# Kernel optimization log

Measured on AMD Instinct MI355X. Metric: run time of the kernel, lower is better.

The kernel has to match this reference:

```python
import jax, jax.numpy as jnp
import numpy as np

N_NODES = 50000      # nodes
N_EDGES = 800000     # edges (avg degree 16)
D = 128              # input_dim == hidden_dim
C = 32               # output_dim (classes)
G = 64               # number of graphs in batch
EPS = 1e-5           # LayerNorm eps (torch default)
NUM_LAYERS = 3


def setup_inputs() -> dict:
    key = jax.random.key(0)
    ks = jax.random.split(key, 12)
    scale = 1.0 / np.sqrt(D)
    x = jax.random.normal(ks[0], (N_NODES, D), dtype=jnp.float32)
    edge_index = jax.random.randint(ks[1], (2, N_EDGES), 0, N_NODES)
    batch = jnp.sort(jax.random.randint(ks[2], (N_NODES,), 0, G))
    # CustomConv params: self-loop linear + message linear, 3 layers stacked
    W_self = jax.random.normal(ks[3], (NUM_LAYERS, D, D), dtype=jnp.float32) * scale
    b_self = jnp.zeros((NUM_LAYERS, D), dtype=jnp.float32)
    W_msg = jax.random.normal(ks[4], (NUM_LAYERS, D, D), dtype=jnp.float32) * scale
    b_msg = jnp.zeros((NUM_LAYERS, D), dtype=jnp.float32)
    # two LayerNorms (after layers 0 and 1)
    ln_g = jnp.ones((2, D), dtype=jnp.float32)
    ln_b = jnp.zeros((2, D), dtype=jnp.float32)
    # post-MP MLP head: Linear(D,D) -> Dropout(identity in eval) -> Linear(D,C)
    W1 = jax.random.normal(ks[5], (D, D), dtype=jnp.float32) * scale
    b1 = jnp.zeros((D,), dtype=jnp.float32)
    W2 = jax.random.normal(ks[6], (D, C), dtype=jnp.float32) * scale
    b2 = jnp.zeros((C,), dtype=jnp.float32)
    return {"x": x, "W_self": W_self, "b_self": b_self, "W_msg": W_msg,
            "b_msg": b_msg, "ln_g": ln_g, "ln_b": ln_b, "W1": W1, "b1": b1,
            "W2": W2, "b2": b2, "edge_index": edge_index, "batch": batch}


def _layer_norm(h, g, b):
    mu = jnp.mean(h, axis=-1, keepdims=True)
    var = jnp.mean(jnp.square(h - mu), axis=-1, keepdims=True)
    return g * (h - mu) * jax.lax.rsqrt(var + EPS) + b


def reference(x, W_self, b_self, W_msg, b_msg, ln_g, ln_b, W1, b1, W2, b2,
              edge_index, batch):
    src, dst = edge_index[0], edge_index[1]
    for i in range(NUM_LAYERS):
        # CustomConv: self linear + sum-aggregated neighbor messages
        msg = x @ W_msg[i] + b_msg[i]                     # [N, D]
        agg = jax.ops.segment_sum(msg[src], dst, num_segments=N_NODES)
        x = x @ W_self[i] + b_self[i] + agg               # [N, D]
        x = jax.nn.relu(x)
        # dropout p=0.25 is identity in eval mode
        if i != NUM_LAYERS - 1:
            x = _layer_norm(x, ln_g[i], ln_b[i])
    # global mean pool over graphs
    sums = jax.ops.segment_sum(x, batch, num_segments=G)          # [G, D]
    cnt = jax.ops.segment_sum(jnp.ones((N_NODES,), x.dtype), batch,
                              num_segments=G)                     # [G]
    pooled = sums / jnp.maximum(cnt, 1.0)[:, None]
    # post-MP head (dropout identity in eval)
    h = pooled @ W1 + b1
    logits = h @ W2 + b2                                          # [G, C]
    return jax.nn.log_softmax(logits, axis=1)
```

## Files before the change

### kernel.cpp

```cpp
#include <hip/hip_runtime.h>
#include <hip/hip_bf16.h>
#include <math.h>

#define N_NODES 50000
#define N_EDGES 800000
#define DIM 128
#define CLS 32
#define NGRAPH 64
#define LN_EPS 1e-5f
#define CSR_CAP (N_EDGES + 8 * N_NODES)
#define NBLK 196
#define ABLK 128
#define EPB (N_EDGES / ABLK)
#define EB_STRIDE 7168
#define LCAP 8192
#define PSPLIT 16

typedef __attribute__((ext_vector_type(8))) short bf16x8;
typedef __attribute__((ext_vector_type(4))) float f32x4;

static __device__ __forceinline__ int lower_bound_i(const int* a, int n, int key) {
    int lo = 0, hi = n;
    while (lo < hi) { int mid = (lo + hi) >> 1; if (a[mid] < key) lo = mid + 1; else hi = mid; }
    return lo;
}


__global__ __launch_bounds__(256) void prep_kernel(
    const float* __restrict__ x, const float* __restrict__ Wself,
    const float* __restrict__ Wmsg, __hip_bfloat16* __restrict__ XbIn,
    __hip_bfloat16* __restrict__ WT,
    int* __restrict__ ecur, float* __restrict__ gsum,
    __hip_bfloat16* __restrict__ padA, __hip_bfloat16* __restrict__ padB,
    __hip_bfloat16* __restrict__ padC, __hip_bfloat16* __restrict__ padD) {
    int i = blockIdx.x * 256 + threadIdx.x;
    if (i < N_NODES * DIM / 2) {
        float2 v = ((const float2*)x)[i];
        ((__hip_bfloat162*)XbIn)[i] = __float22bfloat162_rn(v);
    }
    if (i < 3 * 128 * 256) {
        int l = i / (128 * 256);
        int rem = i - l * (128 * 256);
        int n = rem >> 8;
        int k = rem & 255;
        float v = (k < 128) ? Wself[l * 16384 + k * 128 + n]
                            : Wmsg[l * 16384 + (k - 128) * 128 + n];
        WT[i] = __float2bfloat16(v);
    }
    if (i < NBLK) ecur[i] = i * EB_STRIDE;
    if (i < NGRAPH * DIM) gsum[i] = 0.f;
    if (i < DIM) {
        padA[i] = __float2bfloat16(0.f);
        padB[i] = __float2bfloat16(0.f);
        padC[i] = __float2bfloat16(0.f);
        padD[i] = __float2bfloat16(0.f);
    }
}


__global__ __launch_bounds__(1024) void bucket_kernel(
    const int* __restrict__ esrc, const int* __restrict__ edst,
    int* __restrict__ ecur, int* __restrict__ ebuf) {
    __shared__ int bc[NBLK], bres[NBLK], bcnt[NBLK];
    const int t = threadIdx.x;
    const int e0 = blockIdx.x * EPB;
    if (t < NBLK) bc[t] = 0;
    __syncthreads();
    for (int i = t; i < EPB; i += 1024)
        atomicAdd(&bc[edst[e0 + i] >> 8], 1);
    __syncthreads();
    if (t < NBLK) {
        int c = bc[t];
        int r = (c + 15) & ~15;
        int res = atomicAdd(&ecur[t], r);
        bres[t] = res;
        bcnt[t] = c;
        bc[t] = res;
    }
    __syncthreads();
    for (int i = t; i < EPB; i += 1024) {
        int d = edst[e0 + i];
        int s = esrc[e0 + i];
        int pos = atomicAdd(&bc[d >> 8], 1);
        ebuf[pos] = ((d & 255) << 16) | s;
    }
    __syncthreads();
    if (t < NBLK) {
        int c = bcnt[t], r = (c + 15) & ~15, base = bres[t];
        for (int j = c; j < r; j++) ebuf[base + j] = -1;
    }
}


__global__ __launch_bounds__(1024) void bhist_kernel(
    const int* __restrict__ ebuf, const int* __restrict__ ecur,
    int* __restrict__ counts, int* __restrict__ btot) {
    __shared__ int ncnt[256];
    __shared__ int red[256];
    const int b = blockIdx.x, t = threadIdx.x;
    const int used = ecur[b] - b * EB_STRIDE;
    const int* eb = ebuf + b * EB_STRIDE;
    if (t < 256) ncnt[t] = 0;
    __syncthreads();
    for (int i = t; i < used; i += 1024) {
        int p = eb[i];
        if (p != -1) atomicAdd(&ncnt[p >> 16], 1);
    }
    __syncthreads();
    if (t < 256) {
        int gi = b * 256 + t;
        if (gi < N_NODES) counts[gi] = ncnt[t];
        red[t] = (ncnt[t] + 7) & ~7;
    }
    __syncthreads();
    for (int o = 128; o > 0; o >>= 1) {
        if (t < o) red[t] += red[t + o];
        __syncthreads();
    }
    if (t == 0) btot[b] = red[0];
}


__global__ __launch_bounds__(256) void btot_scan_kernel(const int* __restrict__ btot,
                                                        int* __restrict__ bbase,
                                                        int* __restrict__ off) {
    __shared__ int sd[256];
    int i = threadIdx.x;
    int v = (i < NBLK) ? btot[i] : 0;
    sd[i] = v;
    __syncthreads();
    for (int o = 1; o < 256; o <<= 1) {
        int tv = (i >= o) ? sd[i - o] : 0;
        __syncthreads();
        sd[i] += tv;
        __syncthreads();
    }
    if (i < NBLK) bbase[i] = sd[i] - v;
    if (i == 255) off[N_NODES] = sd[255];
}


__global__ __launch_bounds__(1024) void csr_build_kernel(
    const int* __restrict__ ebuf, const int* __restrict__ ecur,
    const int* __restrict__ counts, const int* __restrict__ bbase,
    int* __restrict__ off, int* __restrict__ csr) {
    __shared__ int cur[256];
    __shared__ int ssc[256];
    __shared__ int lcsr[LCAP];
    const int b = blockIdx.x, t = threadIdx.x;
    const int used = ecur[b] - b * EB_STRIDE;
    const int* eb = ebuf + b * EB_STRIDE;
    const int gbase = bbase[b];
    for (int i = t; i < LCAP; i += 1024) lcsr[i] = N_NODES;
    int myc = 0, mypad = 0;
    const int gi = b * 256 + t;
    if (t < 256) {
        myc = (gi < N_NODES) ? counts[gi] : 0;
        mypad = (myc + 7) & ~7;
        ssc[t] = mypad;
    }
    __syncthreads();
    for (int o = 1; o < 256; o <<= 1) {
        int v = 0;
        if (t < 256 && t >= o) v = ssc[t - o];
        __syncthreads();
        if (t < 256) ssc[t] += v;
        __syncthreads();
    }
    if (t < 256) {
        int eoff = ssc[t] - mypad;
        cur[t] = eoff;
        if (gi < N_NODES) off[gi] = gbase + eoff;
    }
    __syncthreads();
    for (int i = t; i < used; i += 1024) {
        int p = eb[i];
        if (p != -1) {
            int pos = atomicAdd(&cur[p >> 16], 1);
            lcsr[pos] = p & 0xFFFF;
        }
    }
    __syncthreads();
    const int total = ssc[255];
    int4* dst4 = (int4*)(csr + gbase);
    const int4* src4 = (const int4*)lcsr;
    for (int i = t; i < (total >> 2); i += 1024) dst4[i] = src4[i];
}


__global__ __launch_bounds__(256) void agg_kernel(const __hip_bfloat16* __restrict__ Xb,
                                                  const int* __restrict__ off,
                                                  const int* __restrict__ csr,
                                                  __hip_bfloat16* __restrict__ Sb) {
    int wave = threadIdx.x >> 6;
    int lane = threadIdx.x & 63;
    int n = blockIdx.x * 4 + wave;
    if (n >= N_NODES) return;
    int b = off[n], e = off[n + 1];
    float ax = 0.f, ay = 0.f;
    const size_t coloff = (size_t)(lane * 2);
    int base = b;
    for (; base + 16 <= e; base += 16) {
        int idx16 = csr[base + (lane & 15)];
        int s[16];
        unsigned int v[16];
#pragma unroll
        for (int j = 0; j < 16; j++) s[j] = __shfl(idx16, j, 64);
#pragma unroll
        for (int j = 0; j < 16; j++)
            v[j] = *(const unsigned int*)(Xb + (size_t)s[j] * DIM + coloff);
#pragma unroll
        for (int j = 0; j < 16; j++) {
            union { unsigned int u; float f; } lo, hi;
            lo.u = v[j] << 16;
            hi.u = v[j] & 0xffff0000u;
            ax += lo.f;
            ay += hi.f;
        }
    }
    if (base < e) {
        int idx8 = csr[base + (lane & 7)];
        int s[8];
        unsigned int v[8];
#pragma unroll
        for (int j = 0; j < 8; j++) s[j] = __shfl(idx8, j, 64);
#pragma unroll
        for (int j = 0; j < 8; j++)
            v[j] = *(const unsigned int*)(Xb + (size_t)s[j] * DIM + coloff);
#pragma unroll
        for (int j = 0; j < 8; j++) {
            union { unsigned int u; float f; } lo, hi;
            lo.u = v[j] << 16;
            hi.u = v[j] & 0xffff0000u;
            ax += lo.f;
            ay += hi.f;
        }
    }
    ((__hip_bfloat162*)(Sb + (size_t)n * DIM))[lane] =
        __float22bfloat162_rn(make_float2(ax, ay));
}


__global__ __launch_bounds__(256) void layer_mfma_kernel(
    const __hip_bfloat16* __restrict__ Xb, const __hip_bfloat16* __restrict__ Sb,
    const __hip_bfloat16* __restrict__ WT,
    const float* __restrict__ bself, const float* __restrict__ bmsg,
    const int* __restrict__ deg,
    const float* __restrict__ lng, const float* __restrict__ lnb,
    __hip_bfloat16* __restrict__ XoutB, int do_ln) {
    __shared__ __hip_bfloat16 wlds[128 * 136];
    const int tid = threadIdx.x;
    const int w = tid >> 6, lane = tid & 63;
    const int l15 = lane & 15, q = lane >> 4;

    const int row = blockIdx.x * 64 + w * 16 + l15;
    const int rowc = min(row, N_NODES);

    f32x4 acc[8];
#pragma unroll
    for (int ct = 0; ct < 8; ct++) acc[ct] = (f32x4){0.f, 0.f, 0.f, 0.f};

    const __hip_bfloat16* Abase[2] = {Xb, Sb};
    for (int c = 0; c < 2; c++) {
        __syncthreads();
        {
            int n = tid >> 1, h = tid & 1;
            const uint4* src = (const uint4*)(WT + n * 256 + c * 128 + h * 64);
            uint4* dst = (uint4*)(&wlds[n * 136 + h * 64]);
#pragma unroll
            for (int i = 0; i < 8; i++) dst[i] = src[i];
        }
        __syncthreads();
        const __hip_bfloat16* arow = Abase[c] + (size_t)rowc * DIM;
#pragma unroll
        for (int ks = 0; ks < 4; ks++) {
            bf16x8 afrag = *(const bf16x8*)(arow + ks * 32 + q * 8);
#pragma unroll
            for (int ct = 0; ct < 8; ct++) {
                bf16x8 bfrag = *(const bf16x8*)(&wlds[(ct * 16 + l15) * 136 + ks * 32 + q * 8]);
                acc[ct] = __builtin_amdgcn_mfma_f32_16x16x32_bf16(afrag, bfrag, acc[ct], 0, 0, 0);
            }
        }
    }

    const int growbase = blockIdx.x * 64 + w * 16;
#pragma unroll
    for (int r = 0; r < 4; r++) {
        int grow = growbase + q * 4 + r;
        bool valid = grow < N_NODES;
        float dg = valid ? (float)deg[grow] : 0.f;
        float v[8];
        float s1 = 0.f;
#pragma unroll
        for (int ct = 0; ct < 8; ct++) {
            int col = ct * 16 + l15;
            float h = acc[ct][r] + bself[col] + dg * bmsg[col];
            h = fmaxf(h, 0.f);
            v[ct] = h;
            s1 += h;
        }
        if (do_ln) {
#pragma unroll
            for (int m = 1; m < 16; m <<= 1) s1 += __shfl_xor(s1, m, 64);
            float mu = s1 * (1.0f / 128.0f);
            float s2 = 0.f;
#pragma unroll
            for (int ct = 0; ct < 8; ct++) { float d = v[ct] - mu; s2 += d * d; }
#pragma unroll
            for (int m = 1; m < 16; m <<= 1) s2 += __shfl_xor(s2, m, 64);
            float rs = rsqrtf(s2 * (1.0f / 128.0f) + LN_EPS);
#pragma unroll
            for (int ct = 0; ct < 8; ct++) {
                int col = ct * 16 + l15;
                v[ct] = lng[col] * (v[ct] - mu) * rs + lnb[col];
            }
        }
        if (valid) {
#pragma unroll
            for (int ct = 0; ct < 8; ct++) {
                int col = ct * 16 + l15;
                XoutB[(size_t)grow * DIM + col] = __float2bfloat16(v[ct]);
            }
        }
    }
}


__global__ __launch_bounds__(128) void pool_partial_kernel(const __hip_bfloat16* __restrict__ X,
                                                           const int* __restrict__ batch,
                                                           float* __restrict__ gsum) {
    int g = blockIdx.x;
    int s = blockIdx.y;
    int lo = lower_bound_i(batch, N_NODES, g);
    int hi = lower_bound_i(batch, N_NODES, g + 1);
    int len = hi - lo;
    int a = lo + (int)(((long long)len * s) / PSPLIT);
    int b = lo + (int)(((long long)len * (s + 1)) / PSPLIT);
    int c = threadIdx.x;
    float acc = 0.f;
    for (int n = a; n < b; n++) acc += __bfloat162float(X[(size_t)n * DIM + c]);
    if (b > a) atomicAdd(&gsum[g * DIM + c], acc);
}

__global__ __launch_bounds__(128) void head_kernel(
    const float* __restrict__ gsum, const int* __restrict__ batch,
    const float* __restrict__ W1, const float* __restrict__ b1,
    const float* __restrict__ W2, const float* __restrict__ b2,
    float* __restrict__ out) {
    __shared__ float p[128];
    __shared__ float hh[128];
    int g = blockIdx.x;
    int j = threadIdx.x;
    int lo = lower_bound_i(batch, N_NODES, g);
    int hi = lower_bound_i(batch, N_NODES, g + 1);
    float cnt = fmaxf((float)(hi - lo), 1.0f);
    p[j] = gsum[g * DIM + j] / cnt;
    __syncthreads();
    float s = b1[j];
    for (int k = 0; k < DIM; k++) s += p[k] * W1[k * DIM + j];
    hh[j] = s;
    __syncthreads();
    if (j < CLS) {
        float l = b2[j];
        for (int k = 0; k < DIM; k++) l += hh[k] * W2[k * CLS + j];
        float mx = l;
#pragma unroll
        for (int m = 16; m >= 1; m >>= 1) mx = fmaxf(mx, __shfl_xor(mx, m, 64));
        float ex = expf(l - mx);
        float se = ex;
#pragma unroll
        for (int m = 16; m >= 1; m >>= 1) se += __shfl_xor(se, m, 64);
        out[g * CLS + j] = l - mx - logf(se);
    }
}


extern "C" void kernel_launch(void* const* d_in, const int* in_sizes, int n_in,
                              void* d_out, int out_size, void* d_ws, size_t ws_size,
                              hipStream_t stream) {
    (void)in_sizes; (void)n_in; (void)out_size; (void)ws_size;
    const float* x     = (const float*)d_in[0];
    const float* Wself = (const float*)d_in[1];
    const float* bself = (const float*)d_in[2];
    const float* Wmsg  = (const float*)d_in[3];
    const float* bmsg  = (const float*)d_in[4];
    const float* lng   = (const float*)d_in[5];
    const float* lnb   = (const float*)d_in[6];
    const float* W1    = (const float*)d_in[7];
    const float* b1    = (const float*)d_in[8];
    const float* W2    = (const float*)d_in[9];
    const float* b2    = (const float*)d_in[10];
    const int*   ei    = (const int*)d_in[11];
    const int*   batch = (const int*)d_in[12];
    const int* esrc = ei;
    const int* edst = ei + N_EDGES;

    char* w = (char*)d_ws;
    size_t o = 0;
    auto alloc = [&](size_t bytes) { void* p = w + o; o += (bytes + 255) & ~(size_t)255; return p; };
    __hip_bfloat16* XbIn = (__hip_bfloat16*)alloc((size_t)(N_NODES + 1) * DIM * 2);
    __hip_bfloat16* Xb0  = (__hip_bfloat16*)alloc((size_t)(N_NODES + 1) * DIM * 2);
    __hip_bfloat16* Xb1  = (__hip_bfloat16*)alloc((size_t)(N_NODES + 1) * DIM * 2);
    __hip_bfloat16* Sb   = (__hip_bfloat16*)alloc((size_t)(N_NODES + 1) * DIM * 2);
    __hip_bfloat16* WT   = (__hip_bfloat16*)alloc((size_t)3 * 128 * 256 * 2);
    int*   counts = (int*)alloc((size_t)N_NODES * 4);
    int*   offs   = (int*)alloc((size_t)(N_NODES + 1) * 4);
    int*   btot   = (int*)alloc((size_t)NBLK * 4);
    int*   bbase  = (int*)alloc((size_t)NBLK * 4);
    int*   ecur   = (int*)alloc((size_t)NBLK * 4);
    int*   ebuf   = (int*)alloc((size_t)NBLK * EB_STRIDE * 4);
    int*   csr    = (int*)alloc((size_t)CSR_CAP * 4);
    float* gsum   = (float*)alloc((size_t)NGRAPH * DIM * 4);

    prep_kernel<<<(N_NODES * DIM / 2 + 255) / 256, 256, 0, stream>>>(
        x, Wself, Wmsg, XbIn, WT, ecur, gsum,
        XbIn + (size_t)N_NODES * DIM, Xb0 + (size_t)N_NODES * DIM,
        Xb1 + (size_t)N_NODES * DIM, Sb + (size_t)N_NODES * DIM);

    bucket_kernel<<<ABLK, 1024, 0, stream>>>(esrc, edst, ecur, ebuf);
    bhist_kernel<<<NBLK, 1024, 0, stream>>>(ebuf, ecur, counts, btot);
    btot_scan_kernel<<<1, 256, 0, stream>>>(btot, bbase, offs);
    csr_build_kernel<<<NBLK, 1024, 0, stream>>>(ebuf, ecur, counts, bbase, offs, csr);

    const __hip_bfloat16* XbCur = XbIn;
    __hip_bfloat16* bbufs[3] = {Xb0, Xb1, Xb0};
    for (int i = 0; i < 3; i++) {
        agg_kernel<<<(N_NODES + 3) / 4, 256, 0, stream>>>(XbCur, offs, csr, Sb);
        layer_mfma_kernel<<<(N_NODES + 63) / 64, 256, 0, stream>>>(
            XbCur, Sb, WT + (size_t)i * 128 * 256,
            bself + i * DIM, bmsg + i * DIM, counts,
            (i < 2) ? lng + i * DIM : lng, (i < 2) ? lnb + i * DIM : lnb,
            bbufs[i], (i < 2) ? 1 : 0);
        XbCur = bbufs[i];
    }

    pool_partial_kernel<<<dim3(NGRAPH, PSPLIT), 128, 0, stream>>>(bbufs[2], batch, gsum);
    head_kernel<<<NGRAPH, 128, 0, stream>>>(gsum, batch, W1, b1, W2, b2, (float*)d_out);
}
```

Baseline: 294.5 us.

## Store node features in column-group-major layout for cache-local gather

Node feature buffers move from row-major [N,128] to eight column groups of [N+1,16] bf16. The gather kernel now launches 8x more blocks, each handling one 16-column group for 4 nodes, with lanes split across 8 edges at a time and a cross-lane reduction at the end. The aim is to shrink the working set per pass so the gathered rows fit better in L2/LLC. The cost is 32-byte gathers instead of 256-byte rows, more index reloads, the shuffle reduction, and strided A-fragment loads and narrower stores in the MFMA kernel.

```diff
diff --git a/kernel.cpp b/kernel.cpp
--- a/kernel.cpp
+++ b/kernel.cpp
@@ -15,6 +15,7 @@
 #define EB_STRIDE 7168
 #define LCAP 8192
 #define PSPLIT 16
+#define ROWS1 (N_NODES + 1)
 
 typedef __attribute__((ext_vector_type(8))) short bf16x8;
 typedef __attribute__((ext_vector_type(4))) float f32x4;
@@ -28,15 +29,23 @@
 
 __global__ __launch_bounds__(256) void prep_kernel(
     const float* __restrict__ x, const float* __restrict__ Wself,
-    const float* __restrict__ Wmsg, __hip_bfloat16* __restrict__ XbIn,
+    const float* __restrict__ Wmsg, __hip_bfloat16* __restrict__ XcIn,
     __hip_bfloat16* __restrict__ WT,
     int* __restrict__ ecur, float* __restrict__ gsum,
-    __hip_bfloat16* __restrict__ padA, __hip_bfloat16* __restrict__ padB,
-    __hip_bfloat16* __restrict__ padC, __hip_bfloat16* __restrict__ padD) {
+    __hip_bfloat16* __restrict__ padB, __hip_bfloat16* __restrict__ padC,
+    __hip_bfloat16* __restrict__ padD) {
     int i = blockIdx.x * 256 + threadIdx.x;
-    if (i < N_NODES * DIM / 2) {
-        float2 v = ((const float2*)x)[i];
-        ((__hip_bfloat162*)XbIn)[i] = __float22bfloat162_rn(v);
+    if (i < 8 * ROWS1 * 8) {
+        int g = i / (ROWS1 * 8);
+        int rem = i - g * (ROWS1 * 8);
+        int n = rem >> 3;
+        int cp = rem & 7;
+        float2 v = make_float2(0.f, 0.f);
+        if (n < N_NODES) {
+            v.x = x[(size_t)n * DIM + g * 16 + cp * 2];
+            v.y = x[(size_t)n * DIM + g * 16 + cp * 2 + 1];
+        }
+        ((__hip_bfloat162*)XcIn)[(size_t)(g * ROWS1 + n) * 8 + cp] = __float22bfloat162_rn(v);
     }
     if (i < 3 * 128 * 256) {
         int l = i / (128 * 256);
@@ -49,11 +58,12 @@
     }
     if (i < NBLK) ecur[i] = i * EB_STRIDE;
     if (i < NGRAPH * DIM) gsum[i] = 0.f;
-    if (i < DIM) {
-        padA[i] = __float2bfloat16(0.f);
-        padB[i] = __float2bfloat16(0.f);
-        padC[i] = __float2bfloat16(0.f);
-        padD[i] = __float2bfloat16(0.f);
+    if (i < 8 * 16) {
+        int g = i >> 4, c = i & 15;
+        size_t off = (size_t)(g * ROWS1 + N_NODES) * 16 + c;
+        padB[off] = __float2bfloat16(0.f);
+        padC[off] = __float2bfloat16(0.f);
+        padD[off] = __float2bfloat16(0.f);
     }
 }
 
@@ -188,66 +198,60 @@
 }
 
 
-__global__ __launch_bounds__(256) void agg_kernel(const __hip_bfloat16* __restrict__ Xb,
+__global__ __launch_bounds__(256) void agg_kernel(const __hip_bfloat16* __restrict__ Xc,
                                                   const int* __restrict__ off,
                                                   const int* __restrict__ csr,
-                                                  __hip_bfloat16* __restrict__ Sb) {
-    int wave = threadIdx.x >> 6;
-    int lane = threadIdx.x & 63;
-    int n = blockIdx.x * 4 + wave;
+                                                  __hip_bfloat16* __restrict__ Sc) {
+    const int g = blockIdx.x & 7;
+    const int wave = threadIdx.x >> 6;
+    const int lane = threadIdx.x & 63;
+    const int n = (blockIdx.x >> 3) * 4 + wave;
     if (n >= N_NODES) return;
+    const __hip_bfloat16* Xg = Xc + (size_t)g * ROWS1 * 16;
+    const int sub = lane >> 3;
+    const int cl = lane & 7;
     int b = off[n], e = off[n + 1];
     float ax = 0.f, ay = 0.f;
-    const size_t coloff = (size_t)(lane * 2);
     int base = b;
     for (; base + 16 <= e; base += 16) {
         int idx16 = csr[base + (lane & 15)];
-        int s[16];
-        unsigned int v[16];
-#pragma unroll
-        for (int j = 0; j < 16; j++) s[j] = __shfl(idx16, j, 64);
-#pragma unroll
-        for (int j = 0; j < 16; j++)
-            v[j] = *(const unsigned int*)(Xb + (size_t)s[j] * DIM + coloff);
-#pragma unroll
-        for (int j = 0; j < 16; j++) {
-            union { unsigned int u; float f; } lo, hi;
-            lo.u = v[j] << 16;
-            hi.u = v[j] & 0xffff0000u;
-            ax += lo.f;
-            ay += hi.f;
-        }
+        int iA = __shfl(idx16, sub, 64);
+        int iB = __shfl(idx16, sub + 8, 64);
+        unsigned int vA = *(const unsigned int*)(Xg + (size_t)iA * 16 + cl * 2);
+        unsigned int vB = *(const unsigned int*)(Xg + (size_t)iB * 16 + cl * 2);
+        union { unsigned int u; float f; } w0, w1;
+        w0.u = vA << 16; ax += w0.f;
+        w1.u = vA & 0xffff0000u; ay += w1.f;
+        w0.u = vB << 16; ax += w0.f;
+        w1.u = vB & 0xffff0000u; ay += w1.f;
     }
     if (base < e) {
         int idx8 = csr[base + (lane & 7)];
-        int s[8];
-        unsigned int v[8];
-#pragma unroll
-        for (int j = 0; j < 8; j++) s[j] = __shfl(idx8, j, 64);
-#pragma unroll
-        for (int j = 0; j < 8; j++)
-            v[j] = *(const unsigned int*)(Xb + (size_t)s[j] * DIM + coloff);
-#pragma unroll
-        for (int j = 0; j < 8; j++) {
-            union { unsigned int u; float f; } lo, hi;
-            lo.u = v[j] << 16;
-            hi.u = v[j] & 0xffff0000u;
-            ax += lo.f;
-            ay += hi.f;
-        }
-    }
-    ((__hip_bfloat162*)(Sb + (size_t)n * DIM))[lane] =
-        __float22bfloat162_rn(make_float2(ax, ay));
+        int iA = __shfl(idx8, sub, 64);
+        unsigned int vA = *(const unsigned int*)(Xg + (size_t)iA * 16 + cl * 2);
+        union { unsigned int u; float f; } w0, w1;
+        w0.u = vA << 16; ax += w0.f;
+        w1.u = vA & 0xffff0000u; ay += w1.f;
+    }
+#pragma unroll
+    for (int m = 8; m < 64; m <<= 1) {
+        ax += __shfl_xor(ax, m, 64);
+        ay += __shfl_xor(ay, m, 64);
+    }
+    if (lane < 8) {
+        __hip_bfloat162 p = __float22bfloat162_rn(make_float2(ax, ay));
+        ((__hip_bfloat162*)(Sc + (size_t)(g * ROWS1 + n) * 16))[lane] = p;
+    }
 }
 
 
 __global__ __launch_bounds__(256) void layer_mfma_kernel(
-    const __hip_bfloat16* __restrict__ Xb, const __hip_bfloat16* __restrict__ Sb,
+    const __hip_bfloat16* __restrict__ Xc, const __hip_bfloat16* __restrict__ Sc,
     const __hip_bfloat16* __restrict__ WT,
     const float* __restrict__ bself, const float* __restrict__ bmsg,
     const int* __restrict__ deg,
     const float* __restrict__ lng, const float* __restrict__ lnb,
-    __hip_bfloat16* __restrict__ XoutB, int do_ln) {
+    __hip_bfloat16* __restrict__ XoutC, int do_ln) {
     __shared__ __hip_bfloat16 wlds[128 * 136];
     const int tid = threadIdx.x;
     const int w = tid >> 6, lane = tid & 63;
@@ -260,7 +264,7 @@
 #pragma unroll
     for (int ct = 0; ct < 8; ct++) acc[ct] = (f32x4){0.f, 0.f, 0.f, 0.f};
 
-    const __hip_bfloat16* Abase[2] = {Xb, Sb};
+    const __hip_bfloat16* Abase[2] = {Xc, Sc};
     for (int c = 0; c < 2; c++) {
         __syncthreads();
         {
@@ -271,10 +275,11 @@
             for (int i = 0; i < 8; i++) dst[i] = src[i];
         }
         __syncthreads();
-        const __hip_bfloat16* arow = Abase[c] + (size_t)rowc * DIM;
+        const __hip_bfloat16* A = Abase[c];
 #pragma unroll
         for (int ks = 0; ks < 4; ks++) {
-            bf16x8 afrag = *(const bf16x8*)(arow + ks * 32 + q * 8);
+            int gg = 2 * ks + (q >> 1);
+            bf16x8 afrag = *(const bf16x8*)(A + (size_t)(gg * ROWS1 + rowc) * 16 + (q & 1) * 8);
 #pragma unroll
             for (int ct = 0; ct < 8; ct++) {
                 bf16x8 bfrag = *(const bf16x8*)(&wlds[(ct * 16 + l15) * 136 + ks * 32 + q * 8]);
@@ -318,15 +323,14 @@
         if (valid) {
 #pragma unroll
             for (int ct = 0; ct < 8; ct++) {
-                int col = ct * 16 + l15;
-                XoutB[(size_t)grow * DIM + col] = __float2bfloat16(v[ct]);
+                XoutC[(size_t)(ct * ROWS1 + grow) * 16 + l15] = __float2bfloat16(v[ct]);
             }
         }
     }
 }
 
 
-__global__ __launch_bounds__(128) void pool_partial_kernel(const __hip_bfloat16* __restrict__ X,
+__global__ __launch_bounds__(128) void pool_partial_kernel(const __hip_bfloat16* __restrict__ Xc,
                                                            const int* __restrict__ batch,
                                                            float* __restrict__ gsum) {
     int g = blockIdx.x;
@@ -337,8 +341,9 @@
     int a = lo + (int)(((long long)len * s) / PSPLIT);
     int b = lo + (int)(((long long)len * (s + 1)) / PSPLIT);
     int c = threadIdx.x;
+    const __hip_bfloat16* base = Xc + (size_t)(c >> 4) * ROWS1 * 16 + (c & 15);
     float acc = 0.f;
-    for (int n = a; n < b; n++) acc += __bfloat162float(X[(size_t)n * DIM + c]);
+    for (int n = a; n < b; n++) acc += __bfloat162float(base[(size_t)n * 16]);
     if (b > a) atomicAdd(&gsum[g * DIM + c], acc);
 }
 
@@ -398,10 +403,10 @@
     char* w = (char*)d_ws;
     size_t o = 0;
     auto alloc = [&](size_t bytes) { void* p = w + o; o += (bytes + 255) & ~(size_t)255; return p; };
-    __hip_bfloat16* XbIn = (__hip_bfloat16*)alloc((size_t)(N_NODES + 1) * DIM * 2);
-    __hip_bfloat16* Xb0  = (__hip_bfloat16*)alloc((size_t)(N_NODES + 1) * DIM * 2);
-    __hip_bfloat16* Xb1  = (__hip_bfloat16*)alloc((size_t)(N_NODES + 1) * DIM * 2);
-    __hip_bfloat16* Sb   = (__hip_bfloat16*)alloc((size_t)(N_NODES + 1) * DIM * 2);
+    __hip_bfloat16* XcIn = (__hip_bfloat16*)alloc((size_t)8 * ROWS1 * 16 * 2);
+    __hip_bfloat16* Xc0  = (__hip_bfloat16*)alloc((size_t)8 * ROWS1 * 16 * 2);
+    __hip_bfloat16* Xc1  = (__hip_bfloat16*)alloc((size_t)8 * ROWS1 * 16 * 2);
+    __hip_bfloat16* Sc   = (__hip_bfloat16*)alloc((size_t)8 * ROWS1 * 16 * 2);
     __hip_bfloat16* WT   = (__hip_bfloat16*)alloc((size_t)3 * 128 * 256 * 2);
     int*   counts = (int*)alloc((size_t)N_NODES * 4);
     int*   offs   = (int*)alloc((size_t)(N_NODES + 1) * 4);
@@ -412,26 +417,24 @@
     int*   csr    = (int*)alloc((size_t)CSR_CAP * 4);
     float* gsum   = (float*)alloc((size_t)NGRAPH * DIM * 4);
 
-    prep_kernel<<<(N_NODES * DIM / 2 + 255) / 256, 256, 0, stream>>>(
-        x, Wself, Wmsg, XbIn, WT, ecur, gsum,
-        XbIn + (size_t)N_NODES * DIM, Xb0 + (size_t)N_NODES * DIM,
-        Xb1 + (size_t)N_NODES * DIM, Sb + (size_t)N_NODES * DIM);
+    prep_kernel<<<(8 * ROWS1 * 8 + 255) / 256, 256, 0, stream>>>(
+        x, Wself, Wmsg, XcIn, WT, ecur, gsum, Xc0, Xc1, Sc);
 
     bucket_kernel<<<ABLK, 1024, 0, stream>>>(esrc, edst, ecur, ebuf);
     bhist_kernel<<<NBLK, 1024, 0, stream>>>(ebuf, ecur, counts, btot);
     btot_scan_kernel<<<1, 256, 0, stream>>>(btot, bbase, offs);
     csr_build_kernel<<<NBLK, 1024, 0, stream>>>(ebuf, ecur, counts, bbase, offs, csr);
 
-    const __hip_bfloat16* XbCur = XbIn;
-    __hip_bfloat16* bbufs[3] = {Xb0, Xb1, Xb0};
+    const __hip_bfloat16* XcCur = XcIn;
+    __hip_bfloat16* bbufs[3] = {Xc0, Xc1, Xc0};
     for (int i = 0; i < 3; i++) {
-        agg_kernel<<<(N_NODES + 3) / 4, 256, 0, stream>>>(XbCur, offs, csr, Sb);
+        agg_kernel<<<((N_NODES + 3) / 4) * 8, 256, 0, stream>>>(XcCur, offs, csr, Sc);
         layer_mfma_kernel<<<(N_NODES + 63) / 64, 256, 0, stream>>>(
-            XbCur, Sb, WT + (size_t)i * 128 * 256,
+            XcCur, Sc, WT + (size_t)i * 128 * 256,
             bself + i * DIM, bmsg + i * DIM, counts,
             (i < 2) ? lng + i * DIM : lng, (i < 2) ? lnb + i * DIM : lnb,
             bbufs[i], (i < 2) ? 1 : 0);
-        XbCur = bbufs[i];
+        XcCur = bbufs[i];
     }
 
     pool_partial_kernel<<<dim3(NGRAPH, PSPLIT), 128, 0, stream>>>(bbufs[2], batch, gsum);
```

Measured after the change: 460.1 us. 1.56x slower.

## Fuse neighbor aggregation into MFMA layer kernel via LDS staging

Applied to the files above, without the earlier changes.

Each block of the layer kernel now gathers neighbor sums for its 64 rows directly into shared memory, then feeds them to the MFMA loop. This removes the separate aggregation kernel, one launch per layer, and the global round-trip of the aggregated buffer. In exchange, each wave processes 16 nodes serially with far fewer blocks, and extra LDS use may reduce occupancy and latency hiding for the gather.

```diff
diff --git a/kernel.cpp b/kernel.cpp
--- a/kernel.cpp
+++ b/kernel.cpp
@@ -15,6 +15,7 @@
 #define EB_STRIDE 7168
 #define LCAP 8192
 #define PSPLIT 16
+#define ROWS1 (N_NODES + 1)
 
 typedef __attribute__((ext_vector_type(8))) short bf16x8;
 typedef __attribute__((ext_vector_type(4))) float f32x4;
@@ -32,7 +33,7 @@
     __hip_bfloat16* __restrict__ WT,
     int* __restrict__ ecur, float* __restrict__ gsum,
     __hip_bfloat16* __restrict__ padA, __hip_bfloat16* __restrict__ padB,
-    __hip_bfloat16* __restrict__ padC, __hip_bfloat16* __restrict__ padD) {
+    __hip_bfloat16* __restrict__ padC) {
     int i = blockIdx.x * 256 + threadIdx.x;
     if (i < N_NODES * DIM / 2) {
         float2 v = ((const float2*)x)[i];
@@ -53,7 +54,6 @@
         padA[i] = __float2bfloat16(0.f);
         padB[i] = __float2bfloat16(0.f);
         padC[i] = __float2bfloat16(0.f);
-        padD[i] = __float2bfloat16(0.f);
     }
 }
 
@@ -188,79 +188,74 @@
 }
 
 
-__global__ __launch_bounds__(256) void agg_kernel(const __hip_bfloat16* __restrict__ Xb,
-                                                  const int* __restrict__ off,
-                                                  const int* __restrict__ csr,
-                                                  __hip_bfloat16* __restrict__ Sb) {
-    int wave = threadIdx.x >> 6;
-    int lane = threadIdx.x & 63;
-    int n = blockIdx.x * 4 + wave;
-    if (n >= N_NODES) return;
-    int b = off[n], e = off[n + 1];
-    float ax = 0.f, ay = 0.f;
-    const size_t coloff = (size_t)(lane * 2);
-    int base = b;
-    for (; base + 16 <= e; base += 16) {
-        int idx16 = csr[base + (lane & 15)];
-        int s[16];
-        unsigned int v[16];
-#pragma unroll
-        for (int j = 0; j < 16; j++) s[j] = __shfl(idx16, j, 64);
-#pragma unroll
-        for (int j = 0; j < 16; j++)
-            v[j] = *(const unsigned int*)(Xb + (size_t)s[j] * DIM + coloff);
-#pragma unroll
-        for (int j = 0; j < 16; j++) {
-            union { unsigned int u; float f; } lo, hi;
-            lo.u = v[j] << 16;
-            hi.u = v[j] & 0xffff0000u;
-            ax += lo.f;
-            ay += hi.f;
-        }
-    }
-    if (base < e) {
-        int idx8 = csr[base + (lane & 7)];
-        int s[8];
-        unsigned int v[8];
-#pragma unroll
-        for (int j = 0; j < 8; j++) s[j] = __shfl(idx8, j, 64);
-#pragma unroll
-        for (int j = 0; j < 8; j++)
-            v[j] = *(const unsigned int*)(Xb + (size_t)s[j] * DIM + coloff);
-#pragma unroll
-        for (int j = 0; j < 8; j++) {
-            union { unsigned int u; float f; } lo, hi;
-            lo.u = v[j] << 16;
-            hi.u = v[j] & 0xffff0000u;
-            ax += lo.f;
-            ay += hi.f;
-        }
-    }
-    ((__hip_bfloat162*)(Sb + (size_t)n * DIM))[lane] =
-        __float22bfloat162_rn(make_float2(ax, ay));
-}
-
-
-__global__ __launch_bounds__(256) void layer_mfma_kernel(
-    const __hip_bfloat16* __restrict__ Xb, const __hip_bfloat16* __restrict__ Sb,
+__global__ __launch_bounds__(256) void layer_fused_kernel(
+    const __hip_bfloat16* __restrict__ Xb,
+    const int* __restrict__ off, const int* __restrict__ csr,
     const __hip_bfloat16* __restrict__ WT,
     const float* __restrict__ bself, const float* __restrict__ bmsg,
     const int* __restrict__ deg,
     const float* __restrict__ lng, const float* __restrict__ lnb,
     __hip_bfloat16* __restrict__ XoutB, int do_ln) {
     __shared__ __hip_bfloat16 wlds[128 * 136];
+    __shared__ __hip_bfloat16 slds[64 * 136];
     const int tid = threadIdx.x;
     const int w = tid >> 6, lane = tid & 63;
     const int l15 = lane & 15, q = lane >> 4;
-
-    const int row = blockIdx.x * 64 + w * 16 + l15;
-    const int rowc = min(row, N_NODES);
+    const int row0 = blockIdx.x * 64;
+
+    for (int t = 0; t < 16; t++) {
+        int r = w * 16 + t;
+        int n = row0 + r;
+        int b = 0, e = 0;
+        if (n < N_NODES) { b = off[n]; e = off[n + 1]; }
+        float ax = 0.f, ay = 0.f;
+        int base = b;
+        for (; base + 16 <= e; base += 16) {
+            int idx16 = csr[base + (lane & 15)];
+            int s[16];
+            unsigned int v[16];
+#pragma unroll
+            for (int j = 0; j < 16; j++) s[j] = __shfl(idx16, j, 64);
+#pragma unroll
+            for (int j = 0; j < 16; j++)
+                v[j] = *(const unsigned int*)(Xb + (size_t)s[j] * DIM + lane * 2);
+#pragma unroll
+            for (int j = 0; j < 16; j++) {
+                union { unsigned int u; float f; } lo, hi;
+                lo.u = v[j] << 16;
+                hi.u = v[j] & 0xffff0000u;
+                ax += lo.f;
+                ay += hi.f;
+            }
+        }
+        if (base < e) {
+            int idx8 = csr[base + (lane & 7)];
+            int s[8];
+            unsigned int v[8];
+#pragma unroll
+            for (int j = 0; j < 8; j++) s[j] = __shfl(idx8, j, 64);
+#pragma unroll
+            for (int j = 0; j < 8; j++)
+                v[j] = *(const unsigned int*)(Xb + (size_t)s[j] * DIM + lane * 2);
+#pragma unroll
+            for (int j = 0; j < 8; j++) {
+                union { unsigned int u; float f; } lo, hi;
+                lo.u = v[j] << 16;
+                hi.u = v[j] & 0xffff0000u;
+                ax += lo.f;
+                ay += hi.f;
+            }
+        }
+        *(__hip_bfloat162*)(&slds[r * 136 + lane * 2]) =
+            __float22bfloat162_rn(make_float2(ax, ay));
+    }
+
+    const int rowc = min(row0 + w * 16 + l15, N_NODES);
 
     f32x4 acc[8];
 #pragma unroll
     for (int ct = 0; ct < 8; ct++) acc[ct] = (f32x4){0.f, 0.f, 0.f, 0.f};
 
-    const __hip_bfloat16* Abase[2] = {Xb, Sb};
     for (int c = 0; c < 2; c++) {
         __syncthreads();
         {
@@ -271,10 +266,13 @@
             for (int i = 0; i < 8; i++) dst[i] = src[i];
         }
         __syncthreads();
-        const __hip_bfloat16* arow = Abase[c] + (size_t)rowc * DIM;
+        const __hip_bfloat16* arow = Xb + (size_t)rowc * DIM;
+        const __hip_bfloat16* srow = &slds[(w * 16 + l15) * 136];
 #pragma unroll
         for (int ks = 0; ks < 4; ks++) {
-            bf16x8 afrag = *(const bf16x8*)(arow + ks * 32 + q * 8);
+            bf16x8 afrag;
+            if (c == 0) afrag = *(const bf16x8*)(arow + ks * 32 + q * 8);
+            else        afrag = *(const bf16x8*)(srow + ks * 32 + q * 8);
 #pragma unroll
             for (int ct = 0; ct < 8; ct++) {
                 bf16x8 bfrag = *(const bf16x8*)(&wlds[(ct * 16 + l15) * 136 + ks * 32 + q * 8]);
@@ -283,7 +281,7 @@
         }
     }
 
-    const int growbase = blockIdx.x * 64 + w * 16;
+    const int growbase = row0 + w * 16;
 #pragma unroll
     for (int r = 0; r < 4; r++) {
         int grow = growbase + q * 4 + r;
@@ -398,10 +396,9 @@
     char* w = (char*)d_ws;
     size_t o = 0;
     auto alloc = [&](size_t bytes) { void* p = w + o; o += (bytes + 255) & ~(size_t)255; return p; };
-    __hip_bfloat16* XbIn = (__hip_bfloat16*)alloc((size_t)(N_NODES + 1) * DIM * 2);
-    __hip_bfloat16* Xb0  = (__hip_bfloat16*)alloc((size_t)(N_NODES + 1) * DIM * 2);
-    __hip_bfloat16* Xb1  = (__hip_bfloat16*)alloc((size_t)(N_NODES + 1) * DIM * 2);
-    __hip_bfloat16* Sb   = (__hip_bfloat16*)alloc((size_t)(N_NODES + 1) * DIM * 2);
+    __hip_bfloat16* XbIn = (__hip_bfloat16*)alloc((size_t)ROWS1 * DIM * 2);
+    __hip_bfloat16* Xb0  = (__hip_bfloat16*)alloc((size_t)ROWS1 * DIM * 2);
+    __hip_bfloat16* Xb1  = (__hip_bfloat16*)alloc((size_t)ROWS1 * DIM * 2);
     __hip_bfloat16* WT   = (__hip_bfloat16*)alloc((size_t)3 * 128 * 256 * 2);
     int*   counts = (int*)alloc((size_t)N_NODES * 4);
     int*   offs   = (int*)alloc((size_t)(N_NODES + 1) * 4);
@@ -415,7 +412,7 @@
     prep_kernel<<<(N_NODES * DIM / 2 + 255) / 256, 256, 0, stream>>>(
         x, Wself, Wmsg, XbIn, WT, ecur, gsum,
         XbIn + (size_t)N_NODES * DIM, Xb0 + (size_t)N_NODES * DIM,
-        Xb1 + (size_t)N_NODES * DIM, Sb + (size_t)N_NODES * DIM);
+        Xb1 + (size_t)N_NODES * DIM);
 
     bucket_kernel<<<ABLK, 1024, 0, stream>>>(esrc, edst, ecur, ebuf);
     bhist_kernel<<<NBLK, 1024, 0, stream>>>(ebuf, ecur, counts, btot);
@@ -425,9 +422,8 @@
     const __hip_bfloat16* XbCur = XbIn;
     __hip_bfloat16* bbufs[3] = {Xb0, Xb1, Xb0};
     for (int i = 0; i < 3; i++) {
-        agg_kernel<<<(N_NODES + 3) / 4, 256, 0, stream>>>(XbCur, offs, csr, Sb);
-        layer_mfma_kernel<<<(N_NODES + 63) / 64, 256, 0, stream>>>(
-            XbCur, Sb, WT + (size_t)i * 128 * 256,
+        layer_fused_kernel<<<(N_NODES + 63) / 64, 256, 0, stream>>>(
+            XbCur, offs, csr, WT + (size_t)i * 128 * 256,
             bself + i * DIM, bmsg + i * DIM, counts,
             (i < 2) ? lng + i * DIM : lng, (i < 2) ? lnb + i * DIM : lnb,
             bbufs[i], (i < 2) ? 1 : 0);
```

Result: slower. 362.5 us (+23.1%).
